# Performance work log

Measured on AMD Instinct MI355X. Metric: run time of the kernel, lower is better.

## Reference

```python
import jax, jax.numpy as jnp
import numpy as np

B, N = 4, 1024            # batches, atoms per structure
IN_CH, OUT_CH = 16, 16
N_BASIS = 16
MAX_RADIUS = 3.5
BOX_L = 19.7              # cubic lattice constant -> ~24 neighbors/atom
GAMMA = MAX_RADIUS / N_BASIS
N_NORM = 24.0             # avg neighbor count, out /= sqrt(n_norm)


def _build_periodic_edges(seed=0):
    rng = np.random.default_rng(seed)
    pos = rng.uniform(0.0, BOX_L, (B, N, 3)).astype(np.float32)
    shifts = BOX_L * np.array([[i, j, k] for i in (-1, 0, 1)
                               for j in (-1, 0, 1) for k in (-1, 0, 1)],
                              dtype=np.float32)
    src_l, dst_l, vec_l = [], [], []
    r2 = MAX_RADIUS * MAX_RADIUS
    for z in range(B):
        p = pos[z]
        for s in shifts:  # 27 periodic images, chunked to keep memory small
            diff = (p[None, :, :] + s[None, None, :]) - p[:, None, :]  # [a,b,3] = image_b - a
            d2 = (diff * diff).sum(-1)
            a_idx, b_idx = np.nonzero(d2 < r2)
            dst_l.append((z * N + a_idx).astype(np.int32))
            src_l.append((z * N + b_idx).astype(np.int32))
            vec_l.append(diff[a_idx, b_idx])
    edge_src = np.concatenate(src_l)
    edge_dst = np.concatenate(dst_l)
    edge_vec = np.concatenate(vec_l).astype(np.float32)
    # original zeroes self-image displacements with |r| < 1e-10
    self_mask = np.linalg.norm(edge_vec, axis=-1) < 1e-10
    edge_vec[self_mask] = 0.0
    return edge_src, edge_dst, edge_vec


def setup_inputs() -> dict:
    key = jax.random.key(0)
    k1, k2 = jax.random.split(key)
    edge_src, edge_dst, edge_vec = _build_periodic_edges()
    x = jax.random.normal(k1, (B * N, IN_CH), dtype=jnp.float32)
    W = jax.random.normal(k2, (N_BASIS + 3, OUT_CH, IN_CH), dtype=jnp.float32) * 0.1
    return {
        "x": x,
        "W": W,
        "edge_vec": jnp.asarray(edge_vec),
        "edge_src": jnp.asarray(edge_src),
        "edge_dst": jnp.asarray(edge_dst),
    }


def reference(x, W, edge_vec, edge_src, edge_dst):
    # per-edge kernel features: gaussian radial basis + unit direction
    r = jnp.linalg.norm(edge_vec, axis=-1, keepdims=True)            # [E,1]
    centers = jnp.linspace(0.0, MAX_RADIUS, N_BASIS, dtype=x.dtype)
    basis = jnp.exp(-((r - centers) / GAMMA) ** 2)                   # [E,nb]
    rhat = jnp.where(r > 1e-10, edge_vec / jnp.maximum(r, 1e-10), 0.0)
    feat = jnp.concatenate([basis, rhat], axis=-1)                   # [E,nb+3]
    # per-edge kernel eval (kernels = self.kernel(radius) in the original)
    K = jnp.einsum('ef,foi->eoi', feat, W)                           # [E,out,in]
    # per-edge matvec + scatter-add over destination atoms
    msg = jnp.einsum('eoi,ei->eo', K, x[edge_src])                   # [E,out]
    out = jax.ops.segment_sum(msg, edge_dst, num_segments=x.shape[0])
    out = out / jnp.sqrt(jnp.asarray(N_NORM, x.dtype))               # n_norm ** 0.5
    return out.reshape(B, N, OUT_CH)
```

## Files before the change

### kernel.cpp

```cpp
#include <hip/hip_runtime.h>
#include <hip/hip_fp16.h>
#include <math.h>

#define IN_CH 16
#define OUT_CH 16
#define N_BASIS 16
#define N_FEAT 19
#define Y_STRIDE (N_FEAT * OUT_CH)
#define GAMMA_INV (16.0f / 3.5f)
#define CENTER_STEP (3.5f / 15.0f)
#define INV_SQRT_NNORM 0.20412414523193154f
#define APB 16
#define EPB 64

__global__ __launch_bounds__(320) void precompute_y(
    const float* __restrict__ x, const float* __restrict__ W,
    __half* __restrict__ y, float* __restrict__ out, int n_atoms) {
  __shared__ float xs[APB][IN_CH];
  const int t = threadIdx.x;
  const int a0 = blockIdx.x * APB;

  if (t < APB * IN_CH) {
    const int idx = a0 * IN_CH + t;
    const bool ok = idx < n_atoms * IN_CH;
    xs[t >> 4][t & 15] = ok ? x[idx] : 0.0f;
    if (ok) out[idx] = 0.0f;
  }

  float4 w0, w1, w2, w3;
  if (t < Y_STRIDE) {
    const float4* w4 = (const float4*)(W + t * IN_CH);
    w0 = w4[0]; w1 = w4[1]; w2 = w4[2]; w3 = w4[3];
  }
  __syncthreads();

  if (t < Y_STRIDE) {
#pragma unroll
    for (int al = 0; al < APB; ++al) {
      if (a0 + al >= n_atoms) break;
      const float* xv = xs[al];
      float acc = w0.x * xv[0] + w0.y * xv[1] + w0.z * xv[2] + w0.w * xv[3] +
                  w1.x * xv[4] + w1.y * xv[5] + w1.z * xv[6] + w1.w * xv[7] +
                  w2.x * xv[8] + w2.y * xv[9] + w2.z * xv[10] + w2.w * xv[11] +
                  w3.x * xv[12] + w3.y * xv[13] + w3.z * xv[14] + w3.w * xv[15];
      y[(size_t)(a0 + al) * Y_STRIDE + t] = __float2half(acc * INV_SQRT_NNORM);
    }
  }
}

__global__ __launch_bounds__(256) void edge_scatter(
    const __half* __restrict__ y, const float* __restrict__ edge_vec,
    const int* __restrict__ edge_src, const int* __restrict__ edge_dst,
    float* __restrict__ out, int E) {
  __shared__ float feat[EPB][20];
  __shared__ float4 msg4[EPB][4];
  __shared__ int dsts[EPB];

  const int t = threadIdx.x;
  const int h = t & 3;
  const int el = (t >> 2) & 15;
  const int w = t >> 6;
  const int s = w * 16 + el;
  const int e = blockIdx.x * EPB + s;
  const bool valid = (e < E);

  float vx = 0.f, vy = 0.f, vz = 0.f;
  int src = 0;
  if (valid) {
    vx = edge_vec[3 * e + 0];
    vy = edge_vec[3 * e + 1];
    vz = edge_vec[3 * e + 2];
    src = edge_src[e];
    if (h == 0) dsts[s] = edge_dst[e];
  } else if (h == 0) {
    dsts[s] = -1 - s;
  }
  const float r = sqrtf(vx * vx + vy * vy + vz * vz);

#pragma unroll
  for (int j = 0; j < 4; ++j) {
    const float tb = (r - CENTER_STEP * (float)(4 * h + j)) * GAMMA_INV;
    feat[s][4 * h + j] = __expf(-tb * tb);
  }
  if (h < 3) {
    const float inv = (r > 1e-10f) ? (1.0f / r) : 0.0f;
    const float comp = (h == 0) ? vx : ((h == 1) ? vy : vz);
    feat[s][N_BASIS + h] = comp * inv;
  }
  __syncthreads();

  float a0 = 0.f, a1 = 0.f, a2 = 0.f, a3 = 0.f;
  if (valid) {
    const float2* __restrict__ yrow =
        (const float2*)(y + (size_t)src * Y_STRIDE + 4 * h);
#pragma unroll
    for (int f = 0; f < N_FEAT; ++f) {
      const float2 raw = yrow[f * (OUT_CH / 4)];
      const __half2 p0 = *(const __half2*)&raw.x;
      const __half2 p1 = *(const __half2*)&raw.y;
      const float2 v0 = __half22float2(p0);
      const float2 v1 = __half22float2(p1);
      const float ff = feat[s][f];
      a0 += ff * v0.x;
      a1 += ff * v0.y;
      a2 += ff * v1.x;
      a3 += ff * v1.y;
    }
  }
  msg4[s][h] = make_float4(a0, a1, a2, a3);
  __syncthreads();

  const int wb = w * 16;
  const int mydst = dsts[s];
  int leader = el;
#pragma unroll
  for (int k = 0; k < 16; ++k) {
    if (dsts[wb + k] == mydst) { leader = k; break; }
  }
  if (leader == el && mydst >= 0) {
    float s0 = 0.f, s1 = 0.f, s2 = 0.f, s3 = 0.f;
#pragma unroll
    for (int k = 0; k < 16; ++k) {
      if (k >= el && dsts[wb + k] == mydst) {
        const float4 m = msg4[wb + k][h];
        s0 += m.x; s1 += m.y; s2 += m.z; s3 += m.w;
      }
    }
    float* base = &out[mydst * OUT_CH + 4 * h];
    atomicAdd(base + 0, s0);
    atomicAdd(base + 1, s1);
    atomicAdd(base + 2, s2);
    atomicAdd(base + 3, s3);
  }
}

__global__ __launch_bounds__(256) void edge_direct(
    const float* __restrict__ x, const float* __restrict__ W,
    const float* __restrict__ edge_vec, const int* __restrict__ edge_src,
    const int* __restrict__ edge_dst, float* __restrict__ out, int E) {
  __shared__ float Ws[N_FEAT * OUT_CH * IN_CH];
  __shared__ float feat[16][N_FEAT];
  __shared__ float xs[16][IN_CH];

  const int t = threadIdx.x;
  for (int i = t; i < N_FEAT * OUT_CH * IN_CH; i += 256) Ws[i] = W[i];

  const int eg = t >> 4;
  const int o = t & 15;
  const int e = blockIdx.x * 16 + eg;
  const bool valid = (e < E);

  float vx = 0.f, vy = 0.f, vz = 0.f;
  int src = 0, dst = 0;
  if (valid) {
    vx = edge_vec[3 * e + 0];
    vy = edge_vec[3 * e + 1];
    vz = edge_vec[3 * e + 2];
    src = edge_src[e];
    dst = edge_dst[e];
    xs[eg][o] = x[src * IN_CH + o];
  }
  const float r = sqrtf(vx * vx + vy * vy + vz * vz);
  const float tt = (r - CENTER_STEP * (float)o) * GAMMA_INV;
  feat[eg][o] = __expf(-tt * tt);
  if (o < 3) {
    const float inv = (r > 1e-10f) ? (1.0f / r) : 0.0f;
    const float comp = (o == 0) ? vx : ((o == 1) ? vy : vz);
    feat[eg][N_BASIS + o] = comp * inv;
  }
  __syncthreads();

  if (valid) {
    float acc = 0.f;
#pragma unroll
    for (int f = 0; f < N_FEAT; ++f) {
      const float* wrow = &Ws[(f * OUT_CH + o) * IN_CH];
      float dot = 0.f;
#pragma unroll
      for (int i = 0; i < IN_CH; ++i) dot += wrow[i] * xs[eg][i];
      acc += feat[eg][f] * dot;
    }
    atomicAdd(&out[dst * OUT_CH + o], acc * INV_SQRT_NNORM);
  }
}

extern "C" void kernel_launch(void* const* d_in, const int* in_sizes, int n_in,
                              void* d_out, int out_size, void* d_ws,
                              size_t ws_size, hipStream_t stream) {
  const float* x = (const float*)d_in[0];
  const float* W = (const float*)d_in[1];
  const float* edge_vec = (const float*)d_in[2];
  const int* edge_src = (const int*)d_in[3];
  const int* edge_dst = (const int*)d_in[4];
  float* out = (float*)d_out;

  const int E = in_sizes[3];
  const int n_atoms = in_sizes[0] / IN_CH;

  const size_t y_bytes = (size_t)n_atoms * Y_STRIDE * sizeof(__half);
  if (ws_size >= y_bytes) {
    __half* y = (__half*)d_ws;
    precompute_y<<<(n_atoms + APB - 1) / APB, 320, 0, stream>>>(x, W, y, out,
                                                               n_atoms);
    edge_scatter<<<(E + EPB - 1) / EPB, 256, 0, stream>>>(y, edge_vec, edge_src,
                                                          edge_dst, out, E);
  } else {
    hipMemsetAsync(out, 0, (size_t)out_size * sizeof(float), stream);
    edge_direct<<<(E + 15) / 16, 256, 0, stream>>>(x, W, edge_vec, edge_src,
                                                   edge_dst, out, E);
  }
}
```

Before: 76.59 us.

## Fuse y precompute and edge scatter into one cooperative kernel with grid sync

Merges the per-atom y projection and the edge gather/scatter into a single cooperative kernel separated by a grid-wide barrier, launched with one block per 64 edges. This removes one kernel launch and the gap between the two kernels. It also replaces the O(16) leader search with a run-based segmented reduction over consecutive equal destinations. The risk is that a cooperative launch with roughly 1.5k blocks may exceed co-residency limits and fall back to the two-kernel path, and the grid sync has its own cost.

```diff
diff --git a/kernel.cpp b/kernel.cpp
--- a/kernel.cpp
+++ b/kernel.cpp
@@ -1,6 +1,9 @@
 #include <hip/hip_runtime.h>
+#include <hip/hip_cooperative_groups.h>
 #include <hip/hip_fp16.h>
 #include <math.h>
+
+namespace cg = cooperative_groups;
 
 #define IN_CH 16
 #define OUT_CH 16
@@ -13,6 +16,137 @@
 #define APB 16
 #define EPB 64
 
+__global__ __launch_bounds__(256) void fused_conv(
+    const float* __restrict__ x, const float* __restrict__ W,
+    const float* __restrict__ edge_vec, const int* __restrict__ edge_src,
+    const int* __restrict__ edge_dst, __half* __restrict__ y,
+    float* __restrict__ out, int E, int n_atoms, int apb) {
+  __shared__ float xs[4][IN_CH];
+  __shared__ float feat[EPB][20];
+  __shared__ float4 msg4[EPB][4];
+  __shared__ int dsts[EPB];
+
+  const int t = threadIdx.x;
+
+  {
+    const int a0 = blockIdx.x * apb;
+    const int aEnd = min(a0 + apb, n_atoms);
+    if (a0 < aEnd) {
+      const float4* w4a = (const float4*)(W + t * IN_CH);
+      float4 w0 = w4a[0], w1 = w4a[1], w2 = w4a[2], w3 = w4a[3];
+      float4 u0, u1, u2, u3;
+      if (t < Y_STRIDE - 256) {
+        const float4* w4b = (const float4*)(W + (256 + t) * IN_CH);
+        u0 = w4b[0]; u1 = w4b[1]; u2 = w4b[2]; u3 = w4b[3];
+      }
+      for (int base = a0; base < aEnd; base += 4) {
+        const int cnt = min(4, aEnd - base);
+        __syncthreads();
+        if (t < cnt * IN_CH) {
+          xs[t >> 4][t & 15] = x[base * IN_CH + t];
+          out[base * IN_CH + t] = 0.0f;
+        }
+        __syncthreads();
+        for (int al = 0; al < cnt; ++al) {
+          const float* xv = xs[al];
+          float acc =
+              w0.x * xv[0] + w0.y * xv[1] + w0.z * xv[2] + w0.w * xv[3] +
+              w1.x * xv[4] + w1.y * xv[5] + w1.z * xv[6] + w1.w * xv[7] +
+              w2.x * xv[8] + w2.y * xv[9] + w2.z * xv[10] + w2.w * xv[11] +
+              w3.x * xv[12] + w3.y * xv[13] + w3.z * xv[14] + w3.w * xv[15];
+          y[(size_t)(base + al) * Y_STRIDE + t] =
+              __float2half(acc * INV_SQRT_NNORM);
+          if (t < Y_STRIDE - 256) {
+            float acc2 =
+                u0.x * xv[0] + u0.y * xv[1] + u0.z * xv[2] + u0.w * xv[3] +
+                u1.x * xv[4] + u1.y * xv[5] + u1.z * xv[6] + u1.w * xv[7] +
+                u2.x * xv[8] + u2.y * xv[9] + u2.z * xv[10] + u2.w * xv[11] +
+                u3.x * xv[12] + u3.y * xv[13] + u3.z * xv[14] + u3.w * xv[15];
+            y[(size_t)(base + al) * Y_STRIDE + 256 + t] =
+                __float2half(acc2 * INV_SQRT_NNORM);
+          }
+        }
+      }
+    }
+  }
+
+  cg::this_grid().sync();
+
+  const int h = t & 3;
+  const int el = (t >> 2) & 15;
+  const int w = t >> 6;
+  const int s = w * 16 + el;
+  const int e = blockIdx.x * EPB + s;
+  const bool valid = (e < E);
+
+  float vx = 0.f, vy = 0.f, vz = 0.f;
+  int src = 0;
+  if (valid) {
+    vx = edge_vec[3 * e + 0];
+    vy = edge_vec[3 * e + 1];
+    vz = edge_vec[3 * e + 2];
+    src = edge_src[e];
+    if (h == 0) dsts[s] = edge_dst[e];
+  } else if (h == 0) {
+    dsts[s] = -1 - s;
+  }
+  const float r = sqrtf(vx * vx + vy * vy + vz * vz);
+
+#pragma unroll
+  for (int j = 0; j < 4; ++j) {
+    const float tb = (r - CENTER_STEP * (float)(4 * h + j)) * GAMMA_INV;
+    feat[s][4 * h + j] = __expf(-tb * tb);
+  }
+  if (h < 3) {
+    const float inv = (r > 1e-10f) ? (1.0f / r) : 0.0f;
+    const float comp = (h == 0) ? vx : ((h == 1) ? vy : vz);
+    feat[s][N_BASIS + h] = comp * inv;
+  }
+  __syncthreads();
+
+  float a0 = 0.f, a1 = 0.f, a2 = 0.f, a3 = 0.f;
+  if (valid) {
+    const float2* __restrict__ yrow =
+        (const float2*)(y + (size_t)src * Y_STRIDE + 4 * h);
+#pragma unroll
+    for (int f = 0; f < N_FEAT; ++f) {
+      const float2 raw = yrow[f * (OUT_CH / 4)];
+      const float2 v0 = __half22float2(*(const __half2*)&raw.x);
+      const float2 v1 = __half22float2(*(const __half2*)&raw.y);
+      const float ff = feat[s][f];
+      a0 += ff * v0.x;
+      a1 += ff * v0.y;
+      a2 += ff * v1.x;
+      a3 += ff * v1.y;
+    }
+  }
+  msg4[s][h] = make_float4(a0, a1, a2, a3);
+  __syncthreads();
+
+  const int wb = w * 16;
+  const int mydst = dsts[s];
+  const bool lead = (el == 0) || (dsts[s - 1] != mydst);
+  if (lead && mydst >= 0) {
+    float4 m = msg4[s][h];
+    float s0 = m.x, s1 = m.y, s2 = m.z, s3 = m.w;
+    bool run = true;
+#pragma unroll
+    for (int k = 1; k < 16; ++k) {
+      const int kk = el + k;
+      run = run && (kk < 16) && (dsts[wb + kk] == mydst);
+      if (run) {
+        m = msg4[wb + kk][h];
+        s0 += m.x; s1 += m.y; s2 += m.z; s3 += m.w;
+      }
+    }
+    float* base = &out[mydst * OUT_CH + 4 * h];
+    atomicAdd(base + 0, s0);
+    atomicAdd(base + 1, s1);
+    atomicAdd(base + 2, s2);
+    atomicAdd(base + 3, s3);
+  }
+}
+
 __global__ __launch_bounds__(320) void precompute_y(
     const float* __restrict__ x, const float* __restrict__ W,
     __half* __restrict__ y, float* __restrict__ out, int n_atoms) {
@@ -96,10 +230,8 @@
 #pragma unroll
     for (int f = 0; f < N_FEAT; ++f) {
       const float2 raw = yrow[f * (OUT_CH / 4)];
-      const __half2 p0 = *(const __half2*)&raw.x;
-      const __half2 p1 = *(const __half2*)&raw.y;
-      const float2 v0 = __half22float2(p0);
-      const float2 v1 = __half22float2(p1);
+      const float2 v0 = __half22float2(*(const __half2*)&raw.x);
+      const float2 v1 = __half22float2(*(const __half2*)&raw.y);
       const float ff = feat[s][f];
       a0 += ff * v0.x;
       a1 += ff * v0.y;
@@ -112,17 +244,17 @@
 
   const int wb = w * 16;
   const int mydst = dsts[s];
-  int leader = el;
-#pragma unroll
-  for (int k = 0; k < 16; ++k) {
-    if (dsts[wb + k] == mydst) { leader = k; break; }
-  }
-  if (leader == el && mydst >= 0) {
-    float s0 = 0.f, s1 = 0.f, s2 = 0.f, s3 = 0.f;
-#pragma unroll
-    for (int k = 0; k < 16; ++k) {
-      if (k >= el && dsts[wb + k] == mydst) {
-        const float4 m = msg4[wb + k][h];
+  const bool lead = (el == 0) || (dsts[s - 1] != mydst);
+  if (lead && mydst >= 0) {
+    float4 m = msg4[s][h];
+    float s0 = m.x, s1 = m.y, s2 = m.z, s3 = m.w;
+    bool run = true;
+#pragma unroll
+    for (int k = 1; k < 16; ++k) {
+      const int kk = el + k;
+      run = run && (kk < 16) && (dsts[wb + kk] == mydst);
+      if (run) {
+        m = msg4[wb + kk][h];
         s0 += m.x; s1 += m.y; s2 += m.z; s3 += m.w;
       }
     }
@@ -131,56 +263,6 @@
     atomicAdd(base + 1, s1);
     atomicAdd(base + 2, s2);
     atomicAdd(base + 3, s3);
-  }
-}
-
-__global__ __launch_bounds__(256) void edge_direct(
-    const float* __restrict__ x, const float* __restrict__ W,
-    const float* __restrict__ edge_vec, const int* __restrict__ edge_src,
-    const int* __restrict__ edge_dst, float* __restrict__ out, int E) {
-  __shared__ float Ws[N_FEAT * OUT_CH * IN_CH];
-  __shared__ float feat[16][N_FEAT];
-  __shared__ float xs[16][IN_CH];
-
-  const int t = threadIdx.x;
-  for (int i = t; i < N_FEAT * OUT_CH * IN_CH; i += 256) Ws[i] = W[i];
-
-  const int eg = t >> 4;
-  const int o = t & 15;
-  const int e = blockIdx.x * 16 + eg;
-  const bool valid = (e < E);
-
-  float vx = 0.f, vy = 0.f, vz = 0.f;
-  int src = 0, dst = 0;
-  if (valid) {
-    vx = edge_vec[3 * e + 0];
-    vy = edge_vec[3 * e + 1];
-    vz = edge_vec[3 * e + 2];
-    src = edge_src[e];
-    dst = edge_dst[e];
-    xs[eg][o] = x[src * IN_CH + o];
-  }
-  const float r = sqrtf(vx * vx + vy * vy + vz * vz);
-  const float tt = (r - CENTER_STEP * (float)o) * GAMMA_INV;
-  feat[eg][o] = __expf(-tt * tt);
-  if (o < 3) {
-    const float inv = (r > 1e-10f) ? (1.0f / r) : 0.0f;
-    const float comp = (o == 0) ? vx : ((o == 1) ? vy : vz);
-    feat[eg][N_BASIS + o] = comp * inv;
-  }
-  __syncthreads();
-
-  if (valid) {
-    float acc = 0.f;
-#pragma unroll
-    for (int f = 0; f < N_FEAT; ++f) {
-      const float* wrow = &Ws[(f * OUT_CH + o) * IN_CH];
-      float dot = 0.f;
-#pragma unroll
-      for (int i = 0; i < IN_CH; ++i) dot += wrow[i] * xs[eg][i];
-      acc += feat[eg][f] * dot;
-    }
-    atomicAdd(&out[dst * OUT_CH + o], acc * INV_SQRT_NNORM);
   }
 }
 
@@ -194,19 +276,23 @@
   const int* edge_dst = (const int*)d_in[4];
   float* out = (float*)d_out;
 
-  const int E = in_sizes[3];
-  const int n_atoms = in_sizes[0] / IN_CH;
-
-  const size_t y_bytes = (size_t)n_atoms * Y_STRIDE * sizeof(__half);
-  if (ws_size >= y_bytes) {
-    __half* y = (__half*)d_ws;
-    precompute_y<<<(n_atoms + APB - 1) / APB, 320, 0, stream>>>(x, W, y, out,
-                                                               n_atoms);
-    edge_scatter<<<(E + EPB - 1) / EPB, 256, 0, stream>>>(y, edge_vec, edge_src,
-                                                          edge_dst, out, E);
-  } else {
-    hipMemsetAsync(out, 0, (size_t)out_size * sizeof(float), stream);
-    edge_direct<<<(E + 15) / 16, 256, 0, stream>>>(x, W, edge_vec, edge_src,
-                                                   edge_dst, out, E);
-  }
-}
+  int E = in_sizes[3];
+  int n_atoms = in_sizes[0] / IN_CH;
+  __half* y = (__half*)d_ws;
+
+  int nblk = (E + EPB - 1) / EPB;
+  int apb = (n_atoms + nblk - 1) / nblk;
+
+  void* args[] = {(void*)&x,        (void*)&W,   (void*)&edge_vec,
+                  (void*)&edge_src, (void*)&edge_dst, (void*)&y,
+                  (void*)&out,      (void*)&E,   (void*)&n_atoms,
+                  (void*)&apb};
+  hipError_t err = hipLaunchCooperativeKernel(
+      (const void*)fused_conv, dim3(nblk), dim3(256), args, 0, stream);
+  if (err == hipSuccess) return;
+
+  precompute_y<<<(n_atoms + APB - 1) / APB, 320, 0, stream>>>(x, W, y, out,
+                                                              n_atoms);
+  edge_scatter<<<nblk, 256, 0, stream>>>(y, edge_vec, edge_src, edge_dst, out,
+                                         E);
+}
```

Result: slower. 251.5 us (+228.3%).
